# Kernel tuning notes

Measured on AMD Instinct MI355X. Metric: run time of the kernel, lower is better.

Reference implementation:

```python
import jax, jax.numpy as jnp
import numpy as np

B, S, D = 2, 2048, 1024
H, DK, DV = 16, 64, 64
DFF = 4096
EPS_RMS = 1e-6


def setup_inputs() -> dict:
    key = jax.random.key(0)
    ks = jax.random.split(key, 10)
    sc = 0.02
    return {
        "x": jax.random.normal(ks[0], (B, S, D), jnp.float32),
        "w_q": jax.random.normal(ks[1], (D, H * DK), jnp.float32) * sc,
        "w_k": jax.random.normal(ks[2], (D, H * DK), jnp.float32) * sc,
        "w_v": jax.random.normal(ks[3], (D, H * DV), jnp.float32) * sc,
        "w_o": jax.random.normal(ks[4], (H * DV, D), jnp.float32) * sc,
        "w_gate": jax.random.normal(ks[5], (D, DFF), jnp.float32) * sc,
        "w_up": jax.random.normal(ks[6], (D, DFF), jnp.float32) * sc,
        "w_down": jax.random.normal(ks[7], (DFF, D), jnp.float32) * sc,
        "g1": jnp.ones((D,), jnp.float32),
        "g2": jnp.ones((D,), jnp.float32),
    }


def _rmsnorm(x, g):
    var = jnp.mean(jnp.square(x), axis=-1, keepdims=True)
    return x * jax.lax.rsqrt(var + EPS_RMS) * g


def _stable_softmax(s):
    # Faithful to source: exp(x) / (sum exp(x) + 1e-9); fully-masked rows -> 0.
    e = jnp.exp(s)
    return e / (jnp.sum(e, axis=-1, keepdims=True) + 1e-9)


def reference(x, w_q, w_k, w_v, w_o, w_gate, w_up, w_down, g1, g2):
    b, s, d = x.shape
    h = _rmsnorm(x, g1)
    q = (h @ w_q).reshape(b, s, H, DK).transpose(0, 2, 1, 3)  # [B,H,S,DK]
    k = (h @ w_k).reshape(b, s, H, DK).transpose(0, 2, 1, 3)
    v = (h @ w_v).reshape(b, s, H, DV).transpose(0, 2, 1, 3)
    scores = jnp.einsum("bhqd,bhkd->bhqk", q, k) / jnp.sqrt(jnp.asarray(DK, x.dtype))
    # triu with diagonal=0: self and future positions are masked
    mask = jnp.triu(jnp.ones((s, s), bool))
    scores = jnp.where(mask, -jnp.inf, scores)
    attn = _stable_softmax(scores)  # [B,H,S,S]
    av = jnp.einsum("bhqk,bhkd->bhqd", attn, v)
    av = av.transpose(0, 2, 1, 3).reshape(b, s, H * DV)
    x = x + av @ w_o  # residual 1
    h2 = _rmsnorm(x, g2)
    hidden = jax.nn.silu(h2 @ w_gate) * (h2 @ w_up)
    return x + hidden @ w_down  # residual 2
```

## Files before the change

kernel.cpp:

```cpp
#include <hip/hip_runtime.h>
#include <cstdint>
#include <cstddef>

typedef unsigned short u16;
typedef unsigned char u8;
typedef unsigned int u32;
typedef __bf16 bf16x8 __attribute__((ext_vector_type(8)));
typedef float floatx4 __attribute__((ext_vector_type(4)));
typedef float floatx16 __attribute__((ext_vector_type(16)));
typedef int i32x8 __attribute__((ext_vector_type(8)));

#define B_ 2
#define S_ 2048
#define D_ 1024
#define H_ 16
#define DFF_ 4096
#define BS_ 4096

__device__ __forceinline__ u16 f2bf(float f) {
  u32 u = __builtin_bit_cast(u32, f);
  u += 0x7fffu + ((u >> 16) & 1u);
  return (u16)(u >> 16);
}
__device__ __forceinline__ float bf2f(u16 h) {
  u32 u = ((u32)h) << 16;
  return __builtin_bit_cast(float, u);
}

__device__ __forceinline__ u32 cvtpk_bf16(float lo, float hi) {
  u32 r;
  asm("v_cvt_pk_bf16_f32 %0, %1, %2" : "=v"(r) : "v"(lo), "v"(hi));
  return r;
}

__device__ __forceinline__ float fexp2(float x) {
  float r;
  asm("v_exp_f32 %0, %1" : "=v"(r) : "v"(x));
  return r;
}

__device__ __forceinline__ u32 f2e4m3(float f) {
  u32 u = __builtin_bit_cast(u32, f);
  const u32 s = (u >> 24) & 0x80u;
  const u32 au = u & 0x7fffffffu;
  if (au < 0x3c800000u) return s;
  if (au > 0x43e00000u) return s | 0x7eu;
  const u32 lsb = (au >> 20) & 1u;
  const u32 r = au + 0x0007ffffu + lsb;
  const u32 e = (r >> 23) & 0xffu;
  const u32 m = (r >> 20) & 7u;
  return s | (((e - 120u) & 0xfu) << 3) | m;
}

__device__ __forceinline__ void gl_lds16(const void* g, void* l) {
  __builtin_amdgcn_global_load_lds(
      (const __attribute__((address_space(1))) void*)g,
      (__attribute__((address_space(3))) void*)l, 16, 0, 0);
}

__device__ __forceinline__ void xcd_swz(int GX, int GY, int& bx, int& by) {
  int flat = by * GX + bx;
  const int q = (GX * GY) >> 3;
  flat = (flat & 7) * q + (flat >> 3);
  bx = flat % GX;
  by = flat / GX;
}

#define WAITB(N) asm volatile("s_waitcnt vmcnt(" #N ")\n\ts_barrier" ::: "memory")

__global__ void prep_weights(const float* __restrict__ wq, const float* __restrict__ wk,
                             const float* __restrict__ wv, const float* __restrict__ wo,
                             const float* __restrict__ wg, const float* __restrict__ wu,
                             const float* __restrict__ wd,
                             u16* __restrict__ wqkv_t, u16* __restrict__ wo_t,
                             u8* __restrict__ wguf8, u16* __restrict__ wdn_t) {
  __shared__ float tile[32][33];
  const int id = blockIdx.x;
  const float* src;
  u16* dst = nullptr;
  int R, C, bx, by, mode;
  if (id < 3072) {
    const int which = id >> 10, lo = id & 1023;
    src = which == 0 ? wq : (which == 1 ? wk : wv);
    dst = wqkv_t + which * 1024 * 1024;
    R = 1024; C = 1024; bx = lo & 31; by = lo >> 5; mode = 0;
  } else if (id < 4096) {
    const int lo = id - 3072;
    src = wo; dst = wo_t; R = 1024; C = 1024; bx = lo & 31; by = lo >> 5; mode = 0;
  } else if (id < 8192) {
    const int lo = id - 4096;
    src = wg; R = 1024; C = 4096; bx = lo & 127; by = lo >> 7; mode = 1;
  } else if (id < 12288) {
    const int lo = id - 8192;
    src = wu; R = 1024; C = 4096; bx = lo & 127; by = lo >> 7; mode = 2;
  } else {
    const int lo = id - 12288;
    src = wd; dst = wdn_t; R = 4096; C = 1024; bx = lo & 31; by = lo >> 5; mode = 0;
  }
  const int tx = threadIdx.x, ty = threadIdx.y;
  const int c0 = bx * 32, r0 = by * 32;
#pragma unroll
  for (int i = 0; i < 4; i++)
    tile[ty + i * 8][tx] = src[(size_t)(r0 + ty + i * 8) * C + c0 + tx];
  __syncthreads();
  const int sx = ty * 32 + tx;
  const int oci = sx >> 3, cg = (sx & 7) * 4;
  const int oc = c0 + oci;
  const float v0 = tile[cg][oci], v1 = tile[cg + 1][oci];
  const float v2 = tile[cg + 2][oci], v3 = tile[cg + 3][oci];
  if (mode == 0) {
    uint2 o;
    o.x = (u32)f2bf(v0) | ((u32)f2bf(v1) << 16);
    o.y = (u32)f2bf(v2) | ((u32)f2bf(v3) << 16);
    *(uint2*)(dst + (size_t)oc * R + r0 + cg) = o;
  } else {
    const int orow = (oc >> 5) * 64 + (oc & 31) + (mode == 2 ? 32 : 0);
    const u32 p = f2e4m3(v0 * 64.f) | (f2e4m3(v1 * 64.f) << 8) |
                  (f2e4m3(v2 * 64.f) << 16) | (f2e4m3(v3 * 64.f) << 24);
    *(u32*)(wguf8 + (size_t)orow * 1024 + r0 + cg) = p;
  }
}

template <int F8>
__global__ __launch_bounds__(256) void rmsnorm_kernel(const float* __restrict__ x,
                                                      const float* __restrict__ g,
                                                      void* __restrict__ out) {
  const int row = blockIdx.x, t = threadIdx.x;
  const float4 v = ((const float4*)(x + (size_t)row * 1024))[t];
  float ss = v.x * v.x + v.y * v.y + v.z * v.z + v.w * v.w;
#pragma unroll
  for (int off = 32; off > 0; off >>= 1) ss += __shfl_xor(ss, off);
  __shared__ float red[4];
  if ((t & 63) == 0) red[t >> 6] = ss;
  __syncthreads();
  ss = red[0] + red[1] + red[2] + red[3];
  const float inv = rsqrtf(ss * (1.0f / 1024.0f) + 1e-6f);
  const float4 gv = ((const float4*)g)[t];
  const float y0 = v.x * inv * gv.x, y1 = v.y * inv * gv.y;
  const float y2 = v.z * inv * gv.z, y3 = v.w * inv * gv.w;
  if (F8) {
    const u32 p = f2e4m3(y0) | (f2e4m3(y1) << 8) | (f2e4m3(y2) << 16) | (f2e4m3(y3) << 24);
    ((u32*)out)[(size_t)row * 256 + t] = p;
  } else {
    uint2 o;
    o.x = (u32)f2bf(y0) | ((u32)f2bf(y1) << 16);
    o.y = (u32)f2bf(y2) | ((u32)f2bf(y3) << 16);
    ((uint2*)out)[(size_t)row * 256 + t] = o;
  }
}

template <int BN>
__device__ __forceinline__ void bt_step(const u16* Asb, const u16* Bsb,
                                        floatx16 (&acc)[2][BN / 64],
                                        int wm, int wn, int c31, int khalf) {
  constexpr int NTI = BN / 64;
#pragma unroll
  for (int ks = 0; ks < 4; ks++) {
    bf16x8 af[2], bfr[NTI];
#pragma unroll
    for (int mi = 0; mi < 2; mi++) {
      const int row = wm * 64 + mi * 32 + c31;
      const int e = (ks * 2 + khalf) ^ (row & 7);
      af[mi] = *(const bf16x8*)(Asb + row * 64 + e * 8);
    }
#pragma unroll
    for (int ni = 0; ni < NTI; ni++) {
      const int row = wn * (BN / 2) + ni * 32 + c31;
      const int e = (ks * 2 + khalf) ^ (row & 7);
      bfr[ni] = *(const bf16x8*)(Bsb + row * 64 + e * 8);
    }
#pragma unroll
    for (int mi = 0; mi < 2; mi++)
#pragma unroll
      for (int ni = 0; ni < NTI; ni++)
        acc[mi][ni] = __builtin_amdgcn_mfma_f32_32x32x16_bf16(af[mi], bfr[ni],
                                                              acc[mi][ni], 0, 0, 0);
  }
}

template <int SPW>
__device__ __forceinline__ void bt_issue(const u16* (&gsrc)[SPW], u16* const (&ld0)[SPW],
                                         int bufofs) {
#pragma unroll
  for (int i = 0; i < SPW; i++) gl_lds16(gsrc[i], ld0[i] + bufofs);
#pragma unroll
  for (int i = 0; i < SPW; i++) gsrc[i] += 64;
}

template <int BN, int EPI>
__global__ __launch_bounds__(256) void gemm_bt(const u16* __restrict__ A,
                                               const u16* __restrict__ Bt,
                                               void* __restrict__ Cout,
                                               const float* __restrict__ res,
                                               u16* __restrict__ vTout,
                                               int M, int N, int K) {
  constexpr int NTI = BN / 64;
  constexpr int ASZ = 128 * 64;
  constexpr int STRIDE = ASZ + BN * 64;
  constexpr int NBUF = (BN == 64) ? 3 : 2;
  __shared__ u16 SMEM[NBUF * STRIDE];
  constexpr int NSEG = 16 + BN / 8;
  constexpr int SPW = NSEG / 4;
  const int t = threadIdx.x, w = t >> 6, l = t & 63;

  int bx = (int)blockIdx.x, by = (int)blockIdx.y;
  xcd_swz((int)gridDim.x, (int)gridDim.y, bx, by);
  const int m0 = by * 128, n0 = bx * BN;
  const int wm = w >> 1, wn = w & 1;
  const int c31 = l & 31, khalf = l >> 5;

  const u16* gsrc[SPW];
  u16* ld0[SPW];
  {
    const int rl = l >> 3, ch = (l & 7) ^ rl;
#pragma unroll
    for (int i = 0; i < SPW; i++) {
      const int s = w * SPW + i;
      if (s < 16) {
        gsrc[i] = A + (size_t)(m0 + s * 8 + rl) * K + ch * 8;
        ld0[i] = SMEM + s * 512;
      } else {
        gsrc[i] = Bt + (size_t)(n0 + (s - 16) * 8 + rl) * K + ch * 8;
        ld0[i] = SMEM + ASZ + (s - 16) * 512;
      }
    }
  }

  floatx16 acc[2][NTI] = {};

#define BT_STEP(CB) bt_step<BN>(SMEM + (CB)*STRIDE, SMEM + (CB)*STRIDE + ASZ, \
                                acc, wm, wn, c31, khalf)

  if constexpr (BN == 64) {
    bt_issue<SPW>(gsrc, ld0, 0 * STRIDE);
    bt_issue<SPW>(gsrc, ld0, 1 * STRIDE);
    const int NT = K >> 6;
    for (int rep = 0; rep < (NT - 4) / 3; rep++) {
      WAITB(6); bt_issue<SPW>(gsrc, ld0, 2 * STRIDE); BT_STEP(0);
      WAITB(6); bt_issue<SPW>(gsrc, ld0, 0 * STRIDE); BT_STEP(1);
      WAITB(6); bt_issue<SPW>(gsrc, ld0, 1 * STRIDE); BT_STEP(2);
    }
    WAITB(6); bt_issue<SPW>(gsrc, ld0, 2 * STRIDE); BT_STEP(0);
    WAITB(6); bt_issue<SPW>(gsrc, ld0, 0 * STRIDE); BT_STEP(1);
    WAITB(6); BT_STEP(2);
    WAITB(0); BT_STEP(0);
  } else {
    bt_issue<SPW>(gsrc, ld0, 0 * STRIDE);
    bt_issue<SPW>(gsrc, ld0, 1 * STRIDE);
    const int NT = K >> 6;
    for (int kk = 0; kk < NT - 2; kk += 2) {
      WAITB(8); BT_STEP(0);
      __builtin_amdgcn_s_barrier();
      bt_issue<SPW>(gsrc, ld0, 0 * STRIDE);
      WAITB(8); BT_STEP(1);
      __builtin_amdgcn_s_barrier();
      bt_issue<SPW>(gsrc, ld0, 1 * STRIDE);
    }
    WAITB(8); BT_STEP(0);
    WAITB(0); BT_STEP(1);
  }
#undef BT_STEP

  if constexpr (EPI == 3) {
    if (n0 >= 2048) {
#pragma unroll
      for (int mi = 0; mi < 2; mi++)
#pragma unroll
        for (int ni = 0; ni < NTI; ni++) {
          const int col = n0 + wn * (BN / 2) + ni * 32 + c31 - 2048;
          const int hh = col >> 6, dv = col & 63;
          const int rbase = m0 + wm * 64 + mi * 32 + 4 * khalf;
          const int bb = rbase >> 11;
          u16* vp = vTout + (size_t)((bb * 16 + hh) * 64 + dv) * 2048 + (rbase & 2047);
#pragma unroll
          for (int rg = 0; rg < 4; rg++) {
            uint2 pk;
            pk.x = (u32)f2bf(acc[mi][ni][rg * 4 + 0]) |
                   ((u32)f2bf(acc[mi][ni][rg * 4 + 1]) << 16);
            pk.y = (u32)f2bf(acc[mi][ni][rg * 4 + 2]) |
                   ((u32)f2bf(acc[mi][ni][rg * 4 + 3]) << 16);
            *(uint2*)(vp + rg * 8) = pk;
          }
        }
      return;
    }
  }
#pragma unroll
  for (int mi = 0; mi < 2; mi++)
#pragma unroll
    for (int ni = 0; ni < NTI; ni++) {
      const int col = n0 + wn * (BN / 2) + ni * 32 + c31;
#pragma unroll
      for (int reg = 0; reg < 16; reg++) {
        const int row = m0 + wm * 64 + mi * 32 + (reg & 3) + 8 * (reg >> 2) + 4 * khalf;
        const size_t idx = (size_t)row * N + col;
        if (EPI == 1) ((float*)Cout)[idx] = acc[mi][ni][reg] + res[idx];
        else          ((u16*)Cout)[idx] = f2bf(acc[mi][ni][reg]);
      }
    }
}

__device__ __forceinline__ void f8_step(const u8* Asb, const u8* Bsb,
                                        floatx16 (&acc)[2][4],
                                        int wm, int wn, int c31, int hf) {
  i32x8 af[2], bf[4];
#pragma unroll
  for (int mi = 0; mi < 2; mi++) {
    const int r = wm * 64 + mi * 32 + c31;
    const int g = (r >> 1) & 3;
    const uint4 lo = *(const uint4*)(Asb + r * 64 + ((2 * hf) ^ g) * 16);
    const uint4 hi = *(const uint4*)(Asb + r * 64 + ((2 * hf + 1) ^ g) * 16);
    af[mi] = i32x8{(int)lo.x, (int)lo.y, (int)lo.z, (int)lo.w,
                   (int)hi.x, (int)hi.y, (int)hi.z, (int)hi.w};
  }
#pragma unroll
  for (int ni = 0; ni < 4; ni++) {
    const int r = wn * 128 + ni * 32 + c31;
    const int g = (r >> 1) & 3;
    const uint4 lo = *(const uint4*)(Bsb + r * 64 + ((2 * hf) ^ g) * 16);
    const uint4 hi = *(const uint4*)(Bsb + r * 64 + ((2 * hf + 1) ^ g) * 16);
    bf[ni] = i32x8{(int)lo.x, (int)lo.y, (int)lo.z, (int)lo.w,
                   (int)hi.x, (int)hi.y, (int)hi.z, (int)hi.w};
  }
#pragma unroll
  for (int mi = 0; mi < 2; mi++)
#pragma unroll
    for (int ni = 0; ni < 4; ni++)
      acc[mi][ni] = __builtin_amdgcn_mfma_scale_f32_32x32x64_f8f6f4(
          af[mi], bf[ni], acc[mi][ni], 0, 0,
          0, 0x7F7F7F7F,
          0, 0x79797979);
}

__device__ __forceinline__ void f8_issue(const u8* (&gsrc)[6], u8* const (&ld0)[6],
                                         int bufofs) {
#pragma unroll
  for (int i = 0; i < 6; i++) gl_lds16(gsrc[i], ld0[i] + bufofs);
#pragma unroll
  for (int i = 0; i < 6; i++) gsrc[i] += 64;
}

__global__ __launch_bounds__(256) void gemm_f8(const u8* __restrict__ A,
                                               const u8* __restrict__ B,
                                               u16* __restrict__ hid,
                                               int M, int K) {
  constexpr int STRIDE = (128 + 256) * 64;
  __shared__ u8 SMEM[3 * STRIDE];
  const int t = threadIdx.x, w = t >> 6, l = t & 63;
  int bx = (int)blockIdx.x, by = (int)blockIdx.y;
  xcd_swz((int)gridDim.x, (int)gridDim.y, bx, by);
  const int m0 = by * 128, n0 = bx * 256;
  const int wm = w >> 1, wn = w & 1;
  const int c31 = l & 31, hf = l >> 5;

  const u8* gsrc[6];
  u8* ld0[6];
  {
    const int rl = l >> 2, ch = (l & 3) ^ ((l >> 3) & 3);
#pragma unroll
    for (int i = 0; i < 6; i++) {
      const int s = w * 6 + i;
      if (s < 8) {
        gsrc[i] = A + (size_t)(m0 + s * 16 + rl) * K + ch * 16;
        ld0[i] = SMEM + s * 1024;
      } else {
        gsrc[i] = B + (size_t)(n0 + (s - 8) * 16 + rl) * K + ch * 16;
        ld0[i] = SMEM + 8192 + (s - 8) * 1024;
      }
    }
  }

  floatx16 acc[2][4] = {};

#define F8_STEP(CB) f8_step(SMEM + (CB)*STRIDE, SMEM + (CB)*STRIDE + 8192, \
                            acc, wm, wn, c31, hf)

  f8_issue(gsrc, ld0, 0 * STRIDE);
  f8_issue(gsrc, ld0, 1 * STRIDE);
  const int NT = K >> 6;
  for (int rep = 0; rep < (NT - 4) / 3; rep++) {
    WAITB(6); f8_issue(gsrc, ld0, 2 * STRIDE); F8_STEP(0);
    WAITB(6); f8_issue(gsrc, ld0, 0 * STRIDE); F8_STEP(1);
    WAITB(6); f8_issue(gsrc, ld0, 1 * STRIDE); F8_STEP(2);
  }
  WAITB(6); f8_issue(gsrc, ld0, 2 * STRIDE); F8_STEP(0);
  WAITB(6); f8_issue(gsrc, ld0, 0 * STRIDE); F8_STEP(1);
  WAITB(6); F8_STEP(2);
  WAITB(0); F8_STEP(0);
#undef F8_STEP

#pragma unroll
  for (int mi = 0; mi < 2; mi++)
#pragma unroll
    for (int j = 0; j < 2; j++) {
      const int colo = (bx * 4 + wn * 2 + j) * 32 + c31;
#pragma unroll
      for (int reg = 0; reg < 16; reg++) {
        const int row = m0 + wm * 64 + mi * 32 + (reg & 3) + 8 * (reg >> 2) + 4 * hf;
        const float g = acc[mi][2 * j][reg];
        const float u = acc[mi][2 * j + 1][reg];
        hid[(size_t)row * 4096 + colo] = f2bf(g / (1.f + __expf(-g)) * u);
      }
    }
}

__global__ __launch_bounds__(256) void attn_kernel(const u16* __restrict__ qkv,
                                                   const u16* __restrict__ vT,
                                                   u16* __restrict__ av) {
  __shared__ u16 SM[2 * 8192];
  __shared__ u16 Ps[4 * 2048];
  const int t = threadIdx.x, w = t >> 6, l = t & 63;
  const int lrow = l & 15, lk = l >> 4;
  const int bh = blockIdx.x;
  const int b = bh >> 4, h = bh & 15;
  const int qt = 15 - (int)blockIdx.y;
  const int qbase = qt * 128 + w * 32;
  const int ktmax = 2 * qt + 1;
  u16* Pw = Ps + w * 2048;
  const float SC = 0.125f * 1.44269504088896f;

  bf16x8 aq[2][2];
#pragma unroll
  for (int sub = 0; sub < 2; sub++)
#pragma unroll
    for (int half = 0; half < 2; half++)
      aq[sub][half] = *(const bf16x8*)(qkv + (size_t)(b * S_ + qbase + sub * 16 + lrow) * 3072 +
                                       h * 64 + half * 32 + lk * 8);

  const u16* gcur[4];
  int gstep[4], loff[4];
#pragma unroll
  for (int i = 0; i < 4; i++) {
    const int c = w + 4 * i;
    const int half = (c >> 2) & 1, grp = c & 3;
    if (c < 8) {
      gcur[i] = qkv + (size_t)(b * S_ + grp * 16 + (l >> 2)) * 3072 + D_ + h * 64 +
                half * 32 + (l & 3) * 8;
      gstep[i] = 64 * 3072;
      loff[i] = half * 2048 + grp * 512;
    } else {
      gcur[i] = vT + (size_t)(bh * 64 + grp * 16 + (l >> 2)) * S_ + half * 32 + (l & 3) * 8;
      gstep[i] = 64;
      loff[i] = 4096 + half * 2048 + grp * 512;
    }
  }

  floatx4 oacc[2][4] = {};
  float den[2] = {0.f, 0.f};

  int cur = 0;
#pragma unroll
  for (int i = 0; i < 4; i++) { gl_lds16(gcur[i], SM + loff[i]); gcur[i] += gstep[i]; }

  for (int kt = 0; kt <= ktmax; kt++) {
    __syncthreads();
    if (kt < ktmax) {
#pragma unroll
      for (int i = 0; i < 4; i++) {
        gl_lds16(gcur[i], SM + (cur ^ 1) * 8192 + loff[i]);
        gcur[i] += gstep[i];
      }
    }
    const u16* Kbuf = SM + cur * 8192;
    const u16* Vbuf = Kbuf + 4096;

    const bool active = (kt * 64 < qbase + 31);
    if (active) {
      const bool need_mask = (kt * 64 + 64 > qbase);

      bf16x8 bk[4][2];
#pragma unroll
      for (int ct = 0; ct < 4; ct++)
#pragma unroll
        for (int half = 0; half < 2; half++)
          bk[ct][half] = *(const bf16x8*)(Kbuf + half * 2048 + (ct * 16 + lrow) * 32 + lk * 8);

      floatx4 sf[2][4] = {};
      __builtin_amdgcn_s_setprio(1);
#pragma unroll
      for (int sub = 0; sub < 2; sub++)
#pragma unroll
        for (int ct = 0; ct < 4; ct++) {
          sf[sub][ct] = __builtin_amdgcn_mfma_f32_16x16x32_bf16(bk[ct][0], aq[sub][0],
                                                                sf[sub][ct], 0, 0, 0);
          sf[sub][ct] = __builtin_amdgcn_mfma_f32_16x16x32_bf16(bk[ct][1], aq[sub][1],
                                                                sf[sub][ct], 0, 0, 0);
        }
      __builtin_amdgcn_s_setprio(0);

      if (!need_mask) {
#pragma unroll
        for (int sub = 0; sub < 2; sub++) {
          const int prow = sub * 16 + lrow;
#pragma unroll
          for (int ct = 0; ct < 4; ct++) {
            const float p0 = fexp2(sf[sub][ct][0] * SC);
            const float p1 = fexp2(sf[sub][ct][1] * SC);
            const float p2 = fexp2(sf[sub][ct][2] * SC);
            const float p3 = fexp2(sf[sub][ct][3] * SC);
            den[sub] += (p0 + p1) + (p2 + p3);
            uint2 pk;
            pk.x = cvtpk_bf16(p0, p1);
            pk.y = cvtpk_bf16(p2, p3);
            *(uint2*)(Pw + prow * 64 + (((2 * ct + (lk >> 1)) ^ (lrow & 7)) << 3) +
                      (lk & 1) * 4) = pk;
          }
        }
      } else {
#pragma unroll
        for (int sub = 0; sub < 2; sub++) {
          const int qp = qbase + sub * 16 + lrow;
          const int prow = sub * 16 + lrow;
#pragma unroll
          for (int ct = 0; ct < 4; ct++) {
            const int kb = kt * 64 + ct * 16 + lk * 4;
            const float p0 = (kb + 0 < qp) ? fexp2(sf[sub][ct][0] * SC) : 0.f;
            const float p1 = (kb + 1 < qp) ? fexp2(sf[sub][ct][1] * SC) : 0.f;
            const float p2 = (kb + 2 < qp) ? fexp2(sf[sub][ct][2] * SC) : 0.f;
            const float p3 = (kb + 3 < qp) ? fexp2(sf[sub][ct][3] * SC) : 0.f;
            den[sub] += (p0 + p1) + (p2 + p3);
            uint2 pk;
            pk.x = cvtpk_bf16(p0, p1);
            pk.y = cvtpk_bf16(p2, p3);
            *(uint2*)(Pw + prow * 64 + (((2 * ct + (lk >> 1)) ^ (lrow & 7)) << 3) +
                      (lk & 1) * 4) = pk;
          }
        }
      }

      bf16x8 ap[2][2], bv[4][2];
#pragma unroll
      for (int sub = 0; sub < 2; sub++)
#pragma unroll
        for (int kh = 0; kh < 2; kh++) {
          const int prow = sub * 16 + lrow;
          ap[sub][kh] = *(const bf16x8*)(Pw + prow * 64 + (((kh * 4 + lk) ^ (prow & 7)) << 3));
        }
#pragma unroll
      for (int ni = 0; ni < 4; ni++)
#pragma unroll
        for (int kh = 0; kh < 2; kh++)
          bv[ni][kh] = *(const bf16x8*)(Vbuf + kh * 2048 + (ni * 16 + lrow) * 32 + lk * 8);
      __builtin_amdgcn_s_setprio(1);
#pragma unroll
      for (int sub = 0; sub < 2; sub++)
#pragma unroll
        for (int ni = 0; ni < 4; ni++) {
          oacc[sub][ni] = __builtin_amdgcn_mfma_f32_16x16x32_bf16(ap[sub][0], bv[ni][0],
                                                                  oacc[sub][ni], 0, 0, 0);
          oacc[sub][ni] = __builtin_amdgcn_mfma_f32_16x16x32_bf16(ap[sub][1], bv[ni][1],
                                                                  oacc[sub][ni], 0, 0, 0);
        }
      __builtin_amdgcn_s_setprio(0);
    }
    cur ^= 1;
  }

#pragma unroll
  for (int sub = 0; sub < 2; sub++) {
    den[sub] += __shfl_xor(den[sub], 16);
    den[sub] += __shfl_xor(den[sub], 32);
  }
  float dq[2][4];
#pragma unroll
  for (int sub = 0; sub < 2; sub++)
#pragma unroll
    for (int r = 0; r < 4; r++)
      dq[sub][r] = __shfl(den[sub], lk * 4 + r);

#pragma unroll
  for (int sub = 0; sub < 2; sub++)
#pragma unroll
    for (int ni = 0; ni < 4; ni++)
#pragma unroll
      for (int r = 0; r < 4; r++) {
        const int row = qbase + sub * 16 + lk * 4 + r;
        const int col = h * 64 + ni * 16 + lrow;
        av[(size_t)(b * S_ + row) * 1024 + col] = f2bf(oacc[sub][ni][r] / (dq[sub][r] + 1e-9f));
      }
}

#define OFF_WQKV 0u
#define OFF_WO   6291456u
#define OFF_WGU8 8388608u
#define OFF_WDN  16777216u
#define OFF_H1   25165824u
#define OFF_QKV  33554432u
#define OFF_VT   58720256u
#define OFF_AV   67108864u
#define OFF_X1   75497472u
#define OFF_H2F8 92274688u
#define OFF_HID  96468992u

extern "C" void kernel_launch(void* const* d_in, const int* in_sizes, int n_in,
                              void* d_out, int out_size, void* d_ws, size_t ws_size,
                              hipStream_t stream) {
  const float* x      = (const float*)d_in[0];
  const float* w_q    = (const float*)d_in[1];
  const float* w_k    = (const float*)d_in[2];
  const float* w_v    = (const float*)d_in[3];
  const float* w_o    = (const float*)d_in[4];
  const float* w_gate = (const float*)d_in[5];
  const float* w_up   = (const float*)d_in[6];
  const float* w_down = (const float*)d_in[7];
  const float* g1     = (const float*)d_in[8];
  const float* g2     = (const float*)d_in[9];

  char* ws = (char*)d_ws;
  u16* wqkv_t = (u16*)(ws + OFF_WQKV);
  u16* wo_t   = (u16*)(ws + OFF_WO);
  u8*  wguf8  = (u8*)(ws + OFF_WGU8);
  u16* wdn_t  = (u16*)(ws + OFF_WDN);
  u16* h1     = (u16*)(ws + OFF_H1);
  u16* qkv    = (u16*)(ws + OFF_QKV);
  u16* vT     = (u16*)(ws + OFF_VT);
  u16* av     = (u16*)(ws + OFF_AV);
  float* x1   = (float*)(ws + OFF_X1);
  u8*  h2f8   = (u8*)(ws + OFF_H2F8);
  u16* hid    = (u16*)(ws + OFF_HID);
  float* out  = (float*)d_out;

  prep_weights<<<16384, dim3(32, 8), 0, stream>>>(w_q, w_k, w_v, w_o, w_gate, w_up, w_down,
                                                  wqkv_t, wo_t, wguf8, wdn_t);

  rmsnorm_kernel<0><<<BS_, 256, 0, stream>>>(x, g1, h1);
  gemm_bt<128, 3><<<dim3(3072 / 128, BS_ / 128), 256, 0, stream>>>(
      h1, wqkv_t, qkv, nullptr, vT, BS_, 3072, 1024);
  attn_kernel<<<dim3(32, 16), 256, 0, stream>>>(qkv, vT, av);
  gemm_bt<64, 1><<<dim3(1024 / 64, BS_ / 128), 256, 0, stream>>>(
      av, wo_t, x1, x, nullptr, BS_, 1024, 1024);
  rmsnorm_kernel<1><<<BS_, 256, 0, stream>>>(x1, g2, h2f8);
  gemm_f8<<<dim3(8192 / 256, BS_ / 128), 256, 0, stream>>>(h2f8, wguf8, hid, BS_, 1024);
  gemm_bt<64, 1><<<dim3(1024 / 64, BS_ / 128), 256, 0, stream>>>(
      hid, wdn_t, out, x1, nullptr, BS_, 1024, 4096);
}
```

Before: 339.1 us.

## Restructure FP8 gate/up GEMM into 512-thread ping-pong with 16x16x128 MFMA

Rewrites the FP8 gate/up GEMM to use 512-thread blocks with 256x128 tiles and a K-step of 128. It switches to the 16x16x128 scaled MFMA and uses a new XOR-swizzled LDS layout. The main loop is fully unrolled for K=1024 and split into two phases per K-step, each interleaving LDS fragment reads, half of the async global-to-LDS prefetch, barriers and prioritized MFMA bursts. The aim is better overlap of memory and matrix work and fewer LDS stalls. The cost is higher LDS use (144KB, which allows one block per CU) and a schedule hard-coded to K=1024.

```diff
diff --git a/kernel.cpp b/kernel.cpp
--- a/kernel.cpp
+++ b/kernel.cpp
@@ -67,6 +67,9 @@
 }
 
 #define WAITB(N) asm volatile("s_waitcnt vmcnt(" #N ")\n\ts_barrier" ::: "memory")
+
+#define LGKM0 do { asm volatile("s_waitcnt lgkmcnt(0)" ::: "memory"); \
+                   __builtin_amdgcn_sched_barrier(0); } while (0)
 
 __global__ void prep_weights(const float* __restrict__ wq, const float* __restrict__ wk,
                              const float* __restrict__ wv, const float* __restrict__ wo,
@@ -300,108 +303,120 @@
     }
 }
 
-__device__ __forceinline__ void f8_step(const u8* Asb, const u8* Bsb,
-                                        floatx16 (&acc)[2][4],
-                                        int wm, int wn, int c31, int hf) {
-  i32x8 af[2], bf[4];
-#pragma unroll
-  for (int mi = 0; mi < 2; mi++) {
-    const int r = wm * 64 + mi * 32 + c31;
-    const int g = (r >> 1) & 3;
-    const uint4 lo = *(const uint4*)(Asb + r * 64 + ((2 * hf) ^ g) * 16);
-    const uint4 hi = *(const uint4*)(Asb + r * 64 + ((2 * hf + 1) ^ g) * 16);
-    af[mi] = i32x8{(int)lo.x, (int)lo.y, (int)lo.z, (int)lo.w,
-                   (int)hi.x, (int)hi.y, (int)hi.z, (int)hi.w};
-  }
-#pragma unroll
-  for (int ni = 0; ni < 4; ni++) {
-    const int r = wn * 128 + ni * 32 + c31;
-    const int g = (r >> 1) & 3;
-    const uint4 lo = *(const uint4*)(Bsb + r * 64 + ((2 * hf) ^ g) * 16);
-    const uint4 hi = *(const uint4*)(Bsb + r * 64 + ((2 * hf + 1) ^ g) * 16);
-    bf[ni] = i32x8{(int)lo.x, (int)lo.y, (int)lo.z, (int)lo.w,
-                   (int)hi.x, (int)hi.y, (int)hi.z, (int)hi.w};
-  }
-#pragma unroll
-  for (int mi = 0; mi < 2; mi++)
-#pragma unroll
-    for (int ni = 0; ni < 4; ni++)
-      acc[mi][ni] = __builtin_amdgcn_mfma_scale_f32_32x32x64_f8f6f4(
-          af[mi], bf[ni], acc[mi][ni], 0, 0,
-          0, 0x7F7F7F7F,
-          0, 0x79797979);
-}
-
-__device__ __forceinline__ void f8_issue(const u8* (&gsrc)[6], u8* const (&ld0)[6],
-                                         int bufofs) {
-#pragma unroll
-  for (int i = 0; i < 6; i++) gl_lds16(gsrc[i], ld0[i] + bufofs);
-#pragma unroll
-  for (int i = 0; i < 6; i++) gsrc[i] += 64;
-}
-
-__global__ __launch_bounds__(256) void gemm_f8(const u8* __restrict__ A,
-                                               const u8* __restrict__ B,
+__device__ __forceinline__ i32x8 rd32(const u8* base, int r, int l4) {
+  const int key = (r & 7) << 4;
+  const uint4 lo = *(const uint4*)(base + r * 128 + ((l4 * 32) ^ key));
+  const uint4 hi = *(const uint4*)(base + r * 128 + ((l4 * 32 + 16) ^ key));
+  return i32x8{(int)lo.x, (int)lo.y, (int)lo.z, (int)lo.w,
+               (int)hi.x, (int)hi.y, (int)hi.z, (int)hi.w};
+}
+
+__global__ __launch_bounds__(512) void gemm_f8(const u8* __restrict__ A,
+                                               const u8* __restrict__ Bg,
                                                u16* __restrict__ hid,
                                                int M, int K) {
-  constexpr int STRIDE = (128 + 256) * 64;
-  __shared__ u8 SMEM[3 * STRIDE];
+  constexpr int RSZ = 49152;
+  __shared__ u8 SMEM[3 * RSZ];
   const int t = threadIdx.x, w = t >> 6, l = t & 63;
   int bx = (int)blockIdx.x, by = (int)blockIdx.y;
   xcd_swz((int)gridDim.x, (int)gridDim.y, bx, by);
-  const int m0 = by * 128, n0 = bx * 256;
+  const int m0 = by * 256, n0 = bx * 128;
   const int wm = w >> 1, wn = w & 1;
-  const int c31 = l & 31, hf = l >> 5;
+  const int l15 = l & 15, l4 = l >> 4;
 
   const u8* gsrc[6];
-  u8* ld0[6];
+  u32 ldofs[6];
   {
-    const int rl = l >> 2, ch = (l & 3) ^ ((l >> 3) & 3);
+    const int lr = l >> 3, ch = (l & 7) ^ lr;
 #pragma unroll
     for (int i = 0; i < 6; i++) {
       const int s = w * 6 + i;
-      if (s < 8) {
-        gsrc[i] = A + (size_t)(m0 + s * 16 + rl) * K + ch * 16;
-        ld0[i] = SMEM + s * 1024;
+      if (s < 32) {
+        gsrc[i] = A + (size_t)(m0 + s * 8 + lr) * (size_t)K + ch * 16;
+        ldofs[i] = s * 1024u;
       } else {
-        gsrc[i] = B + (size_t)(n0 + (s - 8) * 16 + rl) * K + ch * 16;
-        ld0[i] = SMEM + 8192 + (s - 8) * 1024;
+        gsrc[i] = Bg + (size_t)(n0 + (s - 32) * 8 + lr) * (size_t)K + ch * 16;
+        ldofs[i] = 32768u + (s - 32) * 1024u;
       }
     }
   }
 
-  floatx16 acc[2][4] = {};
-
-#define F8_STEP(CB) f8_step(SMEM + (CB)*STRIDE, SMEM + (CB)*STRIDE + 8192, \
-                            acc, wm, wn, c31, hf)
-
-  f8_issue(gsrc, ld0, 0 * STRIDE);
-  f8_issue(gsrc, ld0, 1 * STRIDE);
-  const int NT = K >> 6;
-  for (int rep = 0; rep < (NT - 4) / 3; rep++) {
-    WAITB(6); f8_issue(gsrc, ld0, 2 * STRIDE); F8_STEP(0);
-    WAITB(6); f8_issue(gsrc, ld0, 0 * STRIDE); F8_STEP(1);
-    WAITB(6); f8_issue(gsrc, ld0, 1 * STRIDE); F8_STEP(2);
-  }
-  WAITB(6); f8_issue(gsrc, ld0, 2 * STRIDE); F8_STEP(0);
-  WAITB(6); f8_issue(gsrc, ld0, 0 * STRIDE); F8_STEP(1);
-  WAITB(6); F8_STEP(2);
-  WAITB(0); F8_STEP(0);
-#undef F8_STEP
-
-#pragma unroll
-  for (int mi = 0; mi < 2; mi++)
-#pragma unroll
-    for (int j = 0; j < 2; j++) {
-      const int colo = (bx * 4 + wn * 2 + j) * 32 + c31;
-#pragma unroll
-      for (int reg = 0; reg < 16; reg++) {
-        const int row = m0 + wm * 64 + mi * 32 + (reg & 3) + 8 * (reg >> 2) + 4 * hf;
-        const float g = acc[mi][2 * j][reg];
-        const float u = acc[mi][2 * j + 1][reg];
-        hid[(size_t)row * 4096 + colo] = f2bf(g / (1.f + __expf(-g)) * u);
+  floatx4 acc[4][4] = {};
+  i32x8 af[4], bf[4];
+
+#define F8_ISSUE(SRHO, HALF)                                         \
+  do {                                                               \
+    _Pragma("unroll") for (int i = (HALF)*3; i < (HALF)*3 + 3; i++) { \
+      gl_lds16(gsrc[i], SMEM + (SRHO)*RSZ + ldofs[i]);               \
+      gsrc[i] += 128;                                                \
+    }                                                                \
+  } while (0)
+
+#define F8_P0(RHO, SRHO, DOST)                                                 \
+  do {                                                                         \
+    const u8* Ra = SMEM + (RHO)*RSZ;                                           \
+    const u8* Rb = Ra + 32768;                                                 \
+    af[0] = rd32(Ra, wm * 64 + 0 * 16 + l15, l4);                              \
+    af[1] = rd32(Ra, wm * 64 + 1 * 16 + l15, l4);                              \
+    af[2] = rd32(Ra, wm * 64 + 2 * 16 + l15, l4);                              \
+    af[3] = rd32(Ra, wm * 64 + 3 * 16 + l15, l4);                              \
+    bf[0] = rd32(Rb, wn * 64 + 0 * 16 + l15, l4);                              \
+    bf[1] = rd32(Rb, wn * 64 + 1 * 16 + l15, l4);                              \
+    if (DOST) F8_ISSUE(SRHO, 0);                                               \
+    __builtin_amdgcn_s_barrier();                                              \
+    LGKM0;                                                                     \
+    __builtin_amdgcn_s_setprio(1);                                             \
+    _Pragma("unroll") for (int ms = 0; ms < 4; ms++)                           \
+      _Pragma("unroll") for (int ns = 0; ns < 2; ns++)                         \
+        acc[ms][ns] = __builtin_amdgcn_mfma_scale_f32_16x16x128_f8f6f4(        \
+            af[ms], bf[ns], acc[ms][ns], 0, 0, 0, 0x7F7F7F7F, 0, 0x79797979);  \
+    __builtin_amdgcn_s_setprio(0);                                             \
+    __builtin_amdgcn_s_barrier();                                              \
+  } while (0)
+
+#define F8_P1(RHO, SRHO, DOST)                                                 \
+  do {                                                                         \
+    const u8* Rb = SMEM + (RHO)*RSZ + 32768;                                   \
+    bf[2] = rd32(Rb, wn * 64 + 2 * 16 + l15, l4);                              \
+    bf[3] = rd32(Rb, wn * 64 + 3 * 16 + l15, l4);                              \
+    if (DOST) F8_ISSUE(SRHO, 1);                                               \
+    __builtin_amdgcn_s_barrier();                                              \
+    LGKM0;                                                                     \
+    __builtin_amdgcn_s_setprio(1);                                             \
+    _Pragma("unroll") for (int ms = 0; ms < 4; ms++)                           \
+      _Pragma("unroll") for (int ns = 2; ns < 4; ns++)                         \
+        acc[ms][ns] = __builtin_amdgcn_mfma_scale_f32_16x16x128_f8f6f4(        \
+            af[ms], bf[ns], acc[ms][ns], 0, 0, 0, 0x7F7F7F7F, 0, 0x79797979);  \
+    __builtin_amdgcn_s_setprio(0);                                             \
+  } while (0)
+
+  F8_ISSUE(0, 0); F8_ISSUE(0, 1);
+  F8_ISSUE(1, 0); F8_ISSUE(1, 1);
+  WAITB(6); F8_P0(0, 2, 1); F8_P1(0, 2, 1);
+  WAITB(6); F8_P0(1, 0, 1); F8_P1(1, 0, 1);
+  WAITB(6); F8_P0(2, 1, 1); F8_P1(2, 1, 1);
+  WAITB(6); F8_P0(0, 2, 1); F8_P1(0, 2, 1);
+  WAITB(6); F8_P0(1, 0, 1); F8_P1(1, 0, 1);
+  WAITB(6); F8_P0(2, 1, 1); F8_P1(2, 1, 1);
+  WAITB(6); F8_P0(0, 0, 0); F8_P1(0, 0, 0);
+  WAITB(0); F8_P0(1, 0, 0); F8_P1(1, 0, 0);
+#undef F8_P0
+#undef F8_P1
+#undef F8_ISSUE
+
+  const int G = bx * 2 + wn;
+#pragma unroll
+  for (int ms = 0; ms < 4; ms++)
+#pragma unroll
+    for (int np = 0; np < 2; np++)
+#pragma unroll
+      for (int reg = 0; reg < 4; reg++) {
+        const int row = m0 + wm * 64 + ms * 16 + l4 * 4 + reg;
+        const int col = G * 32 + np * 16 + l15;
+        const float g = acc[ms][np][reg];
+        const float u = acc[ms][np + 2][reg];
+        hid[(size_t)row * 4096 + col] = f2bf(g / (1.f + __expf(-g)) * u);
       }
-    }
 }
 
 __global__ __launch_bounds__(256) void attn_kernel(const u16* __restrict__ qkv,
@@ -630,7 +645,7 @@
   gemm_bt<64, 1><<<dim3(1024 / 64, BS_ / 128), 256, 0, stream>>>(
       av, wo_t, x1, x, nullptr, BS_, 1024, 1024);
   rmsnorm_kernel<1><<<BS_, 256, 0, stream>>>(x1, g2, h2f8);
-  gemm_f8<<<dim3(8192 / 256, BS_ / 128), 256, 0, stream>>>(h2f8, wguf8, hid, BS_, 1024);
+  gemm_f8<<<dim3(8192 / 128, BS_ / 256), 512, 0, stream>>>(h2f8, wguf8, hid, BS_, 1024);
   gemm_bt<64, 1><<<dim3(1024 / 64, BS_ / 128), 256, 0, stream>>>(
       hid, wdn_t, out, x1, nullptr, BS_, 1024, 4096);
 }
```

Result: slower. 348.3 us (+2.7%).

## Pre-tile FP8 activations for direct fragment loads; pair causal attention tiles per block

Applied to the files above, without the earlier changes.

The second RMSNorm now writes its FP8 output in a tiled layout that matches the MFMA A-fragment order. The FFN gate/up GEMM can then load A straight from global memory into registers and keep only B in LDS. That GEMM moves to 128x128 tiles with a hand-written XCD-aware block mapping and a 64x32 grid. The attention kernel now runs two query tiles per block (tile 15-y and tile y), so every block does a similar amount of causal work with half the grid. Both changes aim to cut LDS traffic and tail imbalance, at the cost of more global loads per block and fewer blocks in flight for attention.

```diff
diff --git a/kernel.cpp b/kernel.cpp
--- a/kernel.cpp
+++ b/kernel.cpp
@@ -140,7 +140,10 @@
   const float y2 = v.z * inv * gv.z, y3 = v.w * inv * gv.w;
   if (F8) {
     const u32 p = f2e4m3(y0) | (f2e4m3(y1) << 8) | (f2e4m3(y2) << 16) | (f2e4m3(y3) << 24);
-    ((u32*)out)[(size_t)row * 256 + t] = p;
+    const int k = t * 4;
+    const u32 ofs = (u32)(((row >> 5) * 16 + (k >> 6)) * 2048 +
+                          ((k >> 5) & 1) * 1024 + (row & 31) * 32 + (k & 31));
+    *(u32*)((u8*)out + ofs) = p;
   } else {
     uint2 o;
     o.x = (u32)f2bf(y0) | ((u32)f2bf(y1) << 16);
@@ -300,108 +303,109 @@
     }
 }
 
-__device__ __forceinline__ void f8_step(const u8* Asb, const u8* Bsb,
-                                        floatx16 (&acc)[2][4],
-                                        int wm, int wn, int c31, int hf) {
-  i32x8 af[2], bf[4];
-#pragma unroll
-  for (int mi = 0; mi < 2; mi++) {
-    const int r = wm * 64 + mi * 32 + c31;
-    const int g = (r >> 1) & 3;
-    const uint4 lo = *(const uint4*)(Asb + r * 64 + ((2 * hf) ^ g) * 16);
-    const uint4 hi = *(const uint4*)(Asb + r * 64 + ((2 * hf + 1) ^ g) * 16);
-    af[mi] = i32x8{(int)lo.x, (int)lo.y, (int)lo.z, (int)lo.w,
-                   (int)hi.x, (int)hi.y, (int)hi.z, (int)hi.w};
-  }
-#pragma unroll
-  for (int ni = 0; ni < 4; ni++) {
-    const int r = wn * 128 + ni * 32 + c31;
-    const int g = (r >> 1) & 3;
-    const uint4 lo = *(const uint4*)(Bsb + r * 64 + ((2 * hf) ^ g) * 16);
-    const uint4 hi = *(const uint4*)(Bsb + r * 64 + ((2 * hf + 1) ^ g) * 16);
-    bf[ni] = i32x8{(int)lo.x, (int)lo.y, (int)lo.z, (int)lo.w,
-                   (int)hi.x, (int)hi.y, (int)hi.z, (int)hi.w};
-  }
-#pragma unroll
-  for (int mi = 0; mi < 2; mi++)
-#pragma unroll
-    for (int ni = 0; ni < 4; ni++)
-      acc[mi][ni] = __builtin_amdgcn_mfma_scale_f32_32x32x64_f8f6f4(
-          af[mi], bf[ni], acc[mi][ni], 0, 0,
-          0, 0x7F7F7F7F,
-          0, 0x79797979);
-}
-
-__device__ __forceinline__ void f8_issue(const u8* (&gsrc)[6], u8* const (&ld0)[6],
-                                         int bufofs) {
-#pragma unroll
-  for (int i = 0; i < 6; i++) gl_lds16(gsrc[i], ld0[i] + bufofs);
-#pragma unroll
-  for (int i = 0; i < 6; i++) gsrc[i] += 64;
-}
-
-__global__ __launch_bounds__(256) void gemm_f8(const u8* __restrict__ A,
-                                               const u8* __restrict__ B,
+__global__ __launch_bounds__(256) void gemm_f8(const u8* __restrict__ Af,
+                                               const u8* __restrict__ Bg,
                                                u16* __restrict__ hid,
                                                int M, int K) {
-  constexpr int STRIDE = (128 + 256) * 64;
-  __shared__ u8 SMEM[3 * STRIDE];
+  constexpr int BSZ = 8192;
+  __shared__ u8 SMEM[3 * BSZ];
   const int t = threadIdx.x, w = t >> 6, l = t & 63;
-  int bx = (int)blockIdx.x, by = (int)blockIdx.y;
-  xcd_swz((int)gridDim.x, (int)gridDim.y, bx, by);
-  const int m0 = by * 128, n0 = bx * 256;
+  int bx, by;
+  {
+    const int flat = (int)blockIdx.y * 64 + (int)blockIdx.x;
+    const int xcd = flat & 7, seq = flat >> 3;
+    const int bxl = seq & 15, byl = (seq >> 4) & 3, bxg = seq >> 6;
+    bx = bxg * 16 + bxl;
+    by = xcd * 4 + byl;
+  }
+  const int m0 = by * 128, n0 = bx * 128;
   const int wm = w >> 1, wn = w & 1;
   const int c31 = l & 31, hf = l >> 5;
 
-  const u8* gsrc[6];
-  u8* ld0[6];
+  const u8* gsrcB[2];
+  u32 ldofsB[2];
   {
     const int rl = l >> 2, ch = (l & 3) ^ ((l >> 3) & 3);
 #pragma unroll
-    for (int i = 0; i < 6; i++) {
-      const int s = w * 6 + i;
-      if (s < 8) {
-        gsrc[i] = A + (size_t)(m0 + s * 16 + rl) * K + ch * 16;
-        ld0[i] = SMEM + s * 1024;
-      } else {
-        gsrc[i] = B + (size_t)(n0 + (s - 8) * 16 + rl) * K + ch * 16;
-        ld0[i] = SMEM + 8192 + (s - 8) * 1024;
-      }
-    }
-  }
-
-  floatx16 acc[2][4] = {};
-
-#define F8_STEP(CB) f8_step(SMEM + (CB)*STRIDE, SMEM + (CB)*STRIDE + 8192, \
-                            acc, wm, wn, c31, hf)
-
-  f8_issue(gsrc, ld0, 0 * STRIDE);
-  f8_issue(gsrc, ld0, 1 * STRIDE);
-  const int NT = K >> 6;
-  for (int rep = 0; rep < (NT - 4) / 3; rep++) {
-    WAITB(6); f8_issue(gsrc, ld0, 2 * STRIDE); F8_STEP(0);
-    WAITB(6); f8_issue(gsrc, ld0, 0 * STRIDE); F8_STEP(1);
-    WAITB(6); f8_issue(gsrc, ld0, 1 * STRIDE); F8_STEP(2);
-  }
-  WAITB(6); f8_issue(gsrc, ld0, 2 * STRIDE); F8_STEP(0);
-  WAITB(6); f8_issue(gsrc, ld0, 0 * STRIDE); F8_STEP(1);
-  WAITB(6); F8_STEP(2);
-  WAITB(0); F8_STEP(0);
-#undef F8_STEP
-
+    for (int i = 0; i < 2; i++) {
+      const int s = w * 2 + i;
+      gsrcB[i] = Bg + (size_t)(n0 + s * 16 + rl) * K + ch * 16;
+      ldofsB[i] = (u32)(s * 1024);
+    }
+  }
+  const u8* Acur[2];
 #pragma unroll
   for (int mi = 0; mi < 2; mi++)
-#pragma unroll
-    for (int j = 0; j < 2; j++) {
-      const int colo = (bx * 4 + wn * 2 + j) * 32 + c31;
-#pragma unroll
-      for (int reg = 0; reg < 16; reg++) {
-        const int row = m0 + wm * 64 + mi * 32 + (reg & 3) + 8 * (reg >> 2) + 4 * hf;
-        const float g = acc[mi][2 * j][reg];
-        const float u = acc[mi][2 * j + 1][reg];
-        hid[(size_t)row * 4096 + colo] = f2bf(g / (1.f + __expf(-g)) * u);
-      }
-    }
+    Acur[mi] = Af + (size_t)((by * 4 + wm * 2 + mi) * 16) * 2048 + l * 32;
+
+  floatx16 acc[2][2] = {};
+  i32x8 afr[3][2];
+
+#define F8_LDA(SL)                                                      \
+  do {                                                                  \
+    _Pragma("unroll") for (int mi = 0; mi < 2; mi++) {                  \
+      const uint4 lo = *(const uint4*)(Acur[mi]);                       \
+      const uint4 hi = *(const uint4*)(Acur[mi] + 16);                  \
+      afr[SL][mi] = i32x8{(int)lo.x, (int)lo.y, (int)lo.z, (int)lo.w,   \
+                          (int)hi.x, (int)hi.y, (int)hi.z, (int)hi.w};  \
+      Acur[mi] += 2048;                                                 \
+    }                                                                   \
+  } while (0)
+
+#define F8_STB(SL)                                              \
+  do {                                                          \
+    _Pragma("unroll") for (int i = 0; i < 2; i++) {             \
+      gl_lds16(gsrcB[i], SMEM + (SL)*BSZ + ldofsB[i]);          \
+      gsrcB[i] += 64;                                           \
+    }                                                           \
+  } while (0)
+
+#define F8_CMP(SL)                                                             \
+  do {                                                                         \
+    const u8* Bs = SMEM + (SL)*BSZ;                                            \
+    i32x8 bfv[2];                                                              \
+    _Pragma("unroll") for (int ni = 0; ni < 2; ni++) {                         \
+      const int r = wn * 64 + ni * 32 + c31;                                   \
+      const int g = (r >> 1) & 3;                                              \
+      const uint4 lo = *(const uint4*)(Bs + r * 64 + ((2 * hf) ^ g) * 16);     \
+      const uint4 hi = *(const uint4*)(Bs + r * 64 + ((2 * hf + 1) ^ g) * 16); \
+      bfv[ni] = i32x8{(int)lo.x, (int)lo.y, (int)lo.z, (int)lo.w,              \
+                      (int)hi.x, (int)hi.y, (int)hi.z, (int)hi.w};             \
+    }                                                                          \
+    _Pragma("unroll") for (int mi = 0; mi < 2; mi++)                           \
+      _Pragma("unroll") for (int ni = 0; ni < 2; ni++)                         \
+        acc[mi][ni] = __builtin_amdgcn_mfma_scale_f32_32x32x64_f8f6f4(         \
+            afr[SL][mi], bfv[ni], acc[mi][ni], 0, 0,                           \
+            0, 0x7F7F7F7F,                                    \
+            0, 0x79797979);         \
+  } while (0)
+
+  F8_LDA(0); F8_STB(0);
+  F8_LDA(1); F8_STB(1);
+  for (int rep = 0; rep < 4; rep++) {
+    WAITB(6); F8_LDA(2); F8_STB(2); F8_CMP(0);
+    WAITB(6); F8_LDA(0); F8_STB(0); F8_CMP(1);
+    WAITB(6); F8_LDA(1); F8_STB(1); F8_CMP(2);
+  }
+  WAITB(6); F8_LDA(2); F8_STB(2); F8_CMP(0);
+  WAITB(6); F8_LDA(0); F8_STB(0); F8_CMP(1);
+  WAITB(6); F8_CMP(2);
+  WAITB(0); F8_CMP(0);
+#undef F8_LDA
+#undef F8_STB
+#undef F8_CMP
+
+#pragma unroll
+  for (int mi = 0; mi < 2; mi++) {
+    const int colo = (bx * 2 + wn) * 32 + c31;
+#pragma unroll
+    for (int reg = 0; reg < 16; reg++) {
+      const int row = m0 + wm * 64 + mi * 32 + (reg & 3) + 8 * (reg >> 2) + 4 * hf;
+      const float g = acc[mi][0][reg];
+      const float u = acc[mi][1][reg];
+      hid[(size_t)row * 4096 + colo] = f2bf(g / (1.f + __expf(-g)) * u);
+    }
+  }
 }
 
 __global__ __launch_bounds__(256) void attn_kernel(const u16* __restrict__ qkv,
@@ -413,171 +417,176 @@
   const int lrow = l & 15, lk = l >> 4;
   const int bh = blockIdx.x;
   const int b = bh >> 4, h = bh & 15;
-  const int qt = 15 - (int)blockIdx.y;
-  const int qbase = qt * 128 + w * 32;
-  const int ktmax = 2 * qt + 1;
   u16* Pw = Ps + w * 2048;
   const float SC = 0.125f * 1.44269504088896f;
 
-  bf16x8 aq[2][2];
-#pragma unroll
-  for (int sub = 0; sub < 2; sub++)
-#pragma unroll
-    for (int half = 0; half < 2; half++)
-      aq[sub][half] = *(const bf16x8*)(qkv + (size_t)(b * S_ + qbase + sub * 16 + lrow) * 3072 +
-                                       h * 64 + half * 32 + lk * 8);
-
-  const u16* gcur[4];
-  int gstep[4], loff[4];
-#pragma unroll
-  for (int i = 0; i < 4; i++) {
-    const int c = w + 4 * i;
-    const int half = (c >> 2) & 1, grp = c & 3;
-    if (c < 8) {
-      gcur[i] = qkv + (size_t)(b * S_ + grp * 16 + (l >> 2)) * 3072 + D_ + h * 64 +
-                half * 32 + (l & 3) * 8;
-      gstep[i] = 64 * 3072;
-      loff[i] = half * 2048 + grp * 512;
-    } else {
-      gcur[i] = vT + (size_t)(bh * 64 + grp * 16 + (l >> 2)) * S_ + half * 32 + (l & 3) * 8;
-      gstep[i] = 64;
-      loff[i] = 4096 + half * 2048 + grp * 512;
-    }
-  }
-
-  floatx4 oacc[2][4] = {};
-  float den[2] = {0.f, 0.f};
-
-  int cur = 0;
-#pragma unroll
-  for (int i = 0; i < 4; i++) { gl_lds16(gcur[i], SM + loff[i]); gcur[i] += gstep[i]; }
-
-  for (int kt = 0; kt <= ktmax; kt++) {
+  for (int pass = 0; pass < 2; pass++) {
+    const int qt = pass == 0 ? (15 - (int)blockIdx.y) : (int)blockIdx.y;
+    const int qbase = qt * 128 + w * 32;
+    const int ktmax = 2 * qt + 1;
+
     __syncthreads();
-    if (kt < ktmax) {
-#pragma unroll
-      for (int i = 0; i < 4; i++) {
-        gl_lds16(gcur[i], SM + (cur ^ 1) * 8192 + loff[i]);
-        gcur[i] += gstep[i];
+
+    bf16x8 aq[2][2];
+#pragma unroll
+    for (int sub = 0; sub < 2; sub++)
+#pragma unroll
+      for (int half = 0; half < 2; half++)
+        aq[sub][half] = *(const bf16x8*)(qkv + (size_t)(b * S_ + qbase + sub * 16 + lrow) * 3072 +
+                                         h * 64 + half * 32 + lk * 8);
+
+    const u16* gcur[4];
+    int gstep[4], loff[4];
+#pragma unroll
+    for (int i = 0; i < 4; i++) {
+      const int c = w + 4 * i;
+      const int half = (c >> 2) & 1, grp = c & 3;
+      if (c < 8) {
+        gcur[i] = qkv + (size_t)(b * S_ + grp * 16 + (l >> 2)) * 3072 + D_ + h * 64 +
+                  half * 32 + (l & 3) * 8;
+        gstep[i] = 64 * 3072;
+        loff[i] = half * 2048 + grp * 512;
+      } else {
+        gcur[i] = vT + (size_t)(bh * 64 + grp * 16 + (l >> 2)) * S_ + half * 32 + (l & 3) * 8;
+        gstep[i] = 64;
+        loff[i] = 4096 + half * 2048 + grp * 512;
       }
     }
-    const u16* Kbuf = SM + cur * 8192;
-    const u16* Vbuf = Kbuf + 4096;
-
-    const bool active = (kt * 64 < qbase + 31);
-    if (active) {
-      const bool need_mask = (kt * 64 + 64 > qbase);
-
-      bf16x8 bk[4][2];
-#pragma unroll
-      for (int ct = 0; ct < 4; ct++)
-#pragma unroll
-        for (int half = 0; half < 2; half++)
-          bk[ct][half] = *(const bf16x8*)(Kbuf + half * 2048 + (ct * 16 + lrow) * 32 + lk * 8);
-
-      floatx4 sf[2][4] = {};
-      __builtin_amdgcn_s_setprio(1);
-#pragma unroll
-      for (int sub = 0; sub < 2; sub++)
-#pragma unroll
-        for (int ct = 0; ct < 4; ct++) {
-          sf[sub][ct] = __builtin_amdgcn_mfma_f32_16x16x32_bf16(bk[ct][0], aq[sub][0],
-                                                                sf[sub][ct], 0, 0, 0);
-          sf[sub][ct] = __builtin_amdgcn_mfma_f32_16x16x32_bf16(bk[ct][1], aq[sub][1],
-                                                                sf[sub][ct], 0, 0, 0);
+
+    floatx4 oacc[2][4] = {};
+    float den[2] = {0.f, 0.f};
+
+    int cur = 0;
+#pragma unroll
+    for (int i = 0; i < 4; i++) { gl_lds16(gcur[i], SM + loff[i]); gcur[i] += gstep[i]; }
+
+    for (int kt = 0; kt <= ktmax; kt++) {
+      __syncthreads();
+      if (kt < ktmax) {
+#pragma unroll
+        for (int i = 0; i < 4; i++) {
+          gl_lds16(gcur[i], SM + (cur ^ 1) * 8192 + loff[i]);
+          gcur[i] += gstep[i];
         }
-      __builtin_amdgcn_s_setprio(0);
-
-      if (!need_mask) {
-#pragma unroll
-        for (int sub = 0; sub < 2; sub++) {
-          const int prow = sub * 16 + lrow;
+      }
+      const u16* Kbuf = SM + cur * 8192;
+      const u16* Vbuf = Kbuf + 4096;
+
+      const bool active = (kt * 64 < qbase + 31);
+      if (active) {
+        const bool need_mask = (kt * 64 + 64 > qbase);
+
+        bf16x8 bk[4][2];
+#pragma unroll
+        for (int ct = 0; ct < 4; ct++)
+#pragma unroll
+          for (int half = 0; half < 2; half++)
+            bk[ct][half] = *(const bf16x8*)(Kbuf + half * 2048 + (ct * 16 + lrow) * 32 + lk * 8);
+
+        floatx4 sf[2][4] = {};
+        __builtin_amdgcn_s_setprio(1);
+#pragma unroll
+        for (int sub = 0; sub < 2; sub++)
 #pragma unroll
           for (int ct = 0; ct < 4; ct++) {
-            const float p0 = fexp2(sf[sub][ct][0] * SC);
-            const float p1 = fexp2(sf[sub][ct][1] * SC);
-            const float p2 = fexp2(sf[sub][ct][2] * SC);
-            const float p3 = fexp2(sf[sub][ct][3] * SC);
-            den[sub] += (p0 + p1) + (p2 + p3);
-            uint2 pk;
-            pk.x = cvtpk_bf16(p0, p1);
-            pk.y = cvtpk_bf16(p2, p3);
-            *(uint2*)(Pw + prow * 64 + (((2 * ct + (lk >> 1)) ^ (lrow & 7)) << 3) +
-                      (lk & 1) * 4) = pk;
+            sf[sub][ct] = __builtin_amdgcn_mfma_f32_16x16x32_bf16(bk[ct][0], aq[sub][0],
+                                                                  sf[sub][ct], 0, 0, 0);
+            sf[sub][ct] = __builtin_amdgcn_mfma_f32_16x16x32_bf16(bk[ct][1], aq[sub][1],
+                                                                  sf[sub][ct], 0, 0, 0);
+          }
+        __builtin_amdgcn_s_setprio(0);
+
+        if (!need_mask) {
+#pragma unroll
+          for (int sub = 0; sub < 2; sub++) {
+            const int prow = sub * 16 + lrow;
+#pragma unroll
+            for (int ct = 0; ct < 4; ct++) {
+              const float p0 = fexp2(sf[sub][ct][0] * SC);
+              const float p1 = fexp2(sf[sub][ct][1] * SC);
+              const float p2 = fexp2(sf[sub][ct][2] * SC);
+              const float p3 = fexp2(sf[sub][ct][3] * SC);
+              den[sub] += (p0 + p1) + (p2 + p3);
+              uint2 pk;
+              pk.x = cvtpk_bf16(p0, p1);
+              pk.y = cvtpk_bf16(p2, p3);
+              *(uint2*)(Pw + prow * 64 + (((2 * ct + (lk >> 1)) ^ (lrow & 7)) << 3) +
+                        (lk & 1) * 4) = pk;
+            }
+          }
+        } else {
+#pragma unroll
+          for (int sub = 0; sub < 2; sub++) {
+            const int qp = qbase + sub * 16 + lrow;
+            const int prow = sub * 16 + lrow;
+#pragma unroll
+            for (int ct = 0; ct < 4; ct++) {
+              const int kb = kt * 64 + ct * 16 + lk * 4;
+              const float p0 = (kb + 0 < qp) ? fexp2(sf[sub][ct][0] * SC) : 0.f;
+              const float p1 = (kb + 1 < qp) ? fexp2(sf[sub][ct][1] * SC) : 0.f;
+              const float p2 = (kb + 2 < qp) ? fexp2(sf[sub][ct][2] * SC) : 0.f;
+              const float p3 = (kb + 3 < qp) ? fexp2(sf[sub][ct][3] * SC) : 0.f;
+              den[sub] += (p0 + p1) + (p2 + p3);
+              uint2 pk;
+              pk.x = cvtpk_bf16(p0, p1);
+              pk.y = cvtpk_bf16(p2, p3);
+              *(uint2*)(Pw + prow * 64 + (((2 * ct + (lk >> 1)) ^ (lrow & 7)) << 3) +
+                        (lk & 1) * 4) = pk;
+            }
           }
         }
-      } else {
-#pragma unroll
-        for (int sub = 0; sub < 2; sub++) {
-          const int qp = qbase + sub * 16 + lrow;
-          const int prow = sub * 16 + lrow;
-#pragma unroll
-          for (int ct = 0; ct < 4; ct++) {
-            const int kb = kt * 64 + ct * 16 + lk * 4;
-            const float p0 = (kb + 0 < qp) ? fexp2(sf[sub][ct][0] * SC) : 0.f;
-            const float p1 = (kb + 1 < qp) ? fexp2(sf[sub][ct][1] * SC) : 0.f;
-            const float p2 = (kb + 2 < qp) ? fexp2(sf[sub][ct][2] * SC) : 0.f;
-            const float p3 = (kb + 3 < qp) ? fexp2(sf[sub][ct][3] * SC) : 0.f;
-            den[sub] += (p0 + p1) + (p2 + p3);
-            uint2 pk;
-            pk.x = cvtpk_bf16(p0, p1);
-            pk.y = cvtpk_bf16(p2, p3);
-            *(uint2*)(Pw + prow * 64 + (((2 * ct + (lk >> 1)) ^ (lrow & 7)) << 3) +
-                      (lk & 1) * 4) = pk;
+
+        bf16x8 ap[2][2], bv[4][2];
+#pragma unroll
+        for (int sub = 0; sub < 2; sub++)
+#pragma unroll
+          for (int kh = 0; kh < 2; kh++) {
+            const int prow = sub * 16 + lrow;
+            ap[sub][kh] = *(const bf16x8*)(Pw + prow * 64 + (((kh * 4 + lk) ^ (prow & 7)) << 3));
           }
+#pragma unroll
+        for (int ni = 0; ni < 4; ni++)
+#pragma unroll
+          for (int kh = 0; kh < 2; kh++)
+            bv[ni][kh] = *(const bf16x8*)(Vbuf + kh * 2048 + (ni * 16 + lrow) * 32 + lk * 8);
+        __builtin_amdgcn_s_setprio(1);
+#pragma unroll
+        for (int sub = 0; sub < 2; sub++)
+#pragma unroll
+          for (int ni = 0; ni < 4; ni++) {
+            oacc[sub][ni] = __builtin_amdgcn_mfma_f32_16x16x32_bf16(ap[sub][0], bv[ni][0],
+                                                                    oacc[sub][ni], 0, 0, 0);
+            oacc[sub][ni] = __builtin_amdgcn_mfma_f32_16x16x32_bf16(ap[sub][1], bv[ni][1],
+                                                                    oacc[sub][ni], 0, 0, 0);
+          }
+        __builtin_amdgcn_s_setprio(0);
+      }
+      cur ^= 1;
+    }
+
+#pragma unroll
+    for (int sub = 0; sub < 2; sub++) {
+      den[sub] += __shfl_xor(den[sub], 16);
+      den[sub] += __shfl_xor(den[sub], 32);
+    }
+    float dq[2][4];
+#pragma unroll
+    for (int sub = 0; sub < 2; sub++)
+#pragma unroll
+      for (int r = 0; r < 4; r++)
+        dq[sub][r] = __shfl(den[sub], lk * 4 + r);
+
+#pragma unroll
+    for (int sub = 0; sub < 2; sub++)
+#pragma unroll
+      for (int ni = 0; ni < 4; ni++)
+#pragma unroll
+        for (int r = 0; r < 4; r++) {
+          const int row = qbase + sub * 16 + lk * 4 + r;
+          const int col = h * 64 + ni * 16 + lrow;
+          av[(size_t)(b * S_ + row) * 1024 + col] = f2bf(oacc[sub][ni][r] / (dq[sub][r] + 1e-9f));
         }
-      }
-
-      bf16x8 ap[2][2], bv[4][2];
-#pragma unroll
-      for (int sub = 0; sub < 2; sub++)
-#pragma unroll
-        for (int kh = 0; kh < 2; kh++) {
-          const int prow = sub * 16 + lrow;
-          ap[sub][kh] = *(const bf16x8*)(Pw + prow * 64 + (((kh * 4 + lk) ^ (prow & 7)) << 3));
-        }
-#pragma unroll
-      for (int ni = 0; ni < 4; ni++)
-#pragma unroll
-        for (int kh = 0; kh < 2; kh++)
-          bv[ni][kh] = *(const bf16x8*)(Vbuf + kh * 2048 + (ni * 16 + lrow) * 32 + lk * 8);
-      __builtin_amdgcn_s_setprio(1);
-#pragma unroll
-      for (int sub = 0; sub < 2; sub++)
-#pragma unroll
-        for (int ni = 0; ni < 4; ni++) {
-          oacc[sub][ni] = __builtin_amdgcn_mfma_f32_16x16x32_bf16(ap[sub][0], bv[ni][0],
-                                                                  oacc[sub][ni], 0, 0, 0);
-          oacc[sub][ni] = __builtin_amdgcn_mfma_f32_16x16x32_bf16(ap[sub][1], bv[ni][1],
-                                                                  oacc[sub][ni], 0, 0, 0);
-        }
-      __builtin_amdgcn_s_setprio(0);
-    }
-    cur ^= 1;
-  }
-
-#pragma unroll
-  for (int sub = 0; sub < 2; sub++) {
-    den[sub] += __shfl_xor(den[sub], 16);
-    den[sub] += __shfl_xor(den[sub], 32);
-  }
-  float dq[2][4];
-#pragma unroll
-  for (int sub = 0; sub < 2; sub++)
-#pragma unroll
-    for (int r = 0; r < 4; r++)
-      dq[sub][r] = __shfl(den[sub], lk * 4 + r);
-
-#pragma unroll
-  for (int sub = 0; sub < 2; sub++)
-#pragma unroll
-    for (int ni = 0; ni < 4; ni++)
-#pragma unroll
-      for (int r = 0; r < 4; r++) {
-        const int row = qbase + sub * 16 + lk * 4 + r;
-        const int col = h * 64 + ni * 16 + lrow;
-        av[(size_t)(b * S_ + row) * 1024 + col] = f2bf(oacc[sub][ni][r] / (dq[sub][r] + 1e-9f));
-      }
+  }
 }
 
 #define OFF_WQKV 0u
@@ -626,11 +635,11 @@
   rmsnorm_kernel<0><<<BS_, 256, 0, stream>>>(x, g1, h1);
   gemm_bt<128, 3><<<dim3(3072 / 128, BS_ / 128), 256, 0, stream>>>(
       h1, wqkv_t, qkv, nullptr, vT, BS_, 3072, 1024);
-  attn_kernel<<<dim3(32, 16), 256, 0, stream>>>(qkv, vT, av);
+  attn_kernel<<<dim3(32, 8), 256, 0, stream>>>(qkv, vT, av);
   gemm_bt<64, 1><<<dim3(1024 / 64, BS_ / 128), 256, 0, stream>>>(
       av, wo_t, x1, x, nullptr, BS_, 1024, 1024);
   rmsnorm_kernel<1><<<BS_, 256, 0, stream>>>(x1, g2, h2f8);
-  gemm_f8<<<dim3(8192 / 256, BS_ / 128), 256, 0, stream>>>(h2f8, wguf8, hid, BS_, 1024);
+  gemm_f8<<<dim3(64, 32), 256, 0, stream>>>(h2f8, wguf8, hid, BS_, 1024);
   gemm_bt<64, 1><<<dim3(1024 / 64, BS_ / 128), 256, 0, stream>>>(
       hid, wdn_t, out, x1, nullptr, BS_, 1024, 4096);
 }
```

Result: no change. 337.3 us, median of 2 (-0.5%).
